# Performance work log

Measured on AMD Instinct MI355X. Metric: run time of the kernel, lower is better.

Reference implementation:

```python
import jax, jax.numpy as jnp
import numpy as np

RATIO = 0.3
BN_EPS = 1e-5
L2_EPS = 1e-8


def setup_inputs() -> dict:
    key = jax.random.key(0)
    ks = jax.random.split(key, 16)
    B, N, D, E = 128, 577, 512, 1024
    H = E // 2  # mlp hidden = 512
    s = lambda k, shp, fan: jax.random.normal(k, shp, dtype=jnp.float32) * (1.0 / np.sqrt(fan))
    return {
        "features": jax.random.normal(ks[0], (B, N, D), dtype=jnp.float32),
        "atten": jax.random.uniform(ks[1], (B, N), dtype=jnp.float32),
        # image_weight_generator: Linear(D,D) -> ReLU -> Linear(D,1)
        "wg_w1": s(ks[2], (D, D), D), "wg_b1": jnp.zeros((D,), jnp.float32),
        "wg_w2": s(ks[3], (D, 1), D), "wg_b2": jnp.zeros((1,), jnp.float32),
        # fc: Linear(D, E)
        "fc_w": s(ks[4], (D, E), D), "fc_b": jnp.zeros((E,), jnp.float32),
        # MLP: Linear(D,H) -> BN(H) -> ReLU -> Linear(H,E)
        "mlp_w0": s(ks[5], (D, H), D), "mlp_b0": jnp.zeros((H,), jnp.float32),
        "bn_g": jnp.ones((H,), jnp.float32), "bn_b": jnp.zeros((H,), jnp.float32),
        "mlp_w1": s(ks[6], (H, E), H), "mlp_b1": jnp.zeros((E,), jnp.float32),
    }


def reference(features, atten, wg_w1, wg_b1, wg_w2, wg_b2, fc_w, fc_b,
              mlp_w0, mlp_b0, bn_g, bn_b, mlp_w1, mlp_b1):
    k = int((atten.shape[1] - 1) * RATIO)  # static: int(576*0.3)=172
    # weight-generator MLP -> per-token scalar weights [B, N]
    h = jax.nn.relu(jnp.einsum('bnd,de->bne', features, wg_w1) + wg_b1)
    w = (jnp.einsum('bnd,do->bno', h, wg_w2) + wg_b2)[..., 0]
    w = w.at[:, 0].set(-jnp.inf)  # mask CLS token
    w = jax.nn.softmax(w, axis=1)
    # top-k token selection (sorted indices), batched gather
    _, idx = jax.lax.top_k(w, k)                      # [B, k]
    idx = jnp.sort(idx, axis=1)
    sel = jnp.take_along_axis(features, idx[:, :, None], axis=1)  # [B, k, D]
    # l2norm over feature dim
    norm = jnp.sqrt(jnp.sum(sel * sel, axis=-1, keepdims=True)) + L2_EPS
    sel = sel / norm
    # fc in half precision (original: fc(selected_tokens.half()))
    feats = (sel.astype(jnp.float16) @ fc_w.astype(jnp.float16)
             + fc_b.astype(jnp.float16))              # [B, k, E] fp16
    # MLP with training-mode BatchNorm over flattened (B*k) dim
    B, K, D = sel.shape
    x = sel.reshape(B * K, D) @ mlp_w0 + mlp_b0       # [B*k, H]
    mean = jnp.mean(x, axis=0)
    var = jnp.mean((x - mean) ** 2, axis=0)
    x = (x - mean) * jax.lax.rsqrt(var + BN_EPS) * bn_g + bn_b
    x = jax.nn.relu(x)
    x = (x @ mlp_w1 + mlp_b1).reshape(B, K, -1)       # [B, k, E]
    return (x + feats.astype(jnp.float32)).astype(jnp.float32)
```

## Files before the change

### kernel.cpp

```cpp
#include <hip/hip_runtime.h>
#include <hip/hip_fp16.h>
#include <math.h>

#define B_    128
#define NTOK  577
#define D_    512
#define E_    1024
#define KSEL  172
#define M_WG  (B_*NTOK)
#define M_SEL (B_*KSEL)

typedef float f32x4 __attribute__((ext_vector_type(4)));
typedef short s16x8 __attribute__((ext_vector_type(8)));
typedef short s16x4 __attribute__((ext_vector_type(4)));

__device__ __forceinline__ unsigned short bf16_rne(float x) {
    unsigned u = __float_as_uint(x);
    u += 0x7FFFu + ((u >> 16) & 1u);
    return (unsigned short)(u >> 16);
}
__device__ __forceinline__ float bf16f(unsigned short h) {
    return __uint_as_float(((unsigned)h) << 16);
}

__global__ void zero_kernel(float* __restrict__ w, float* __restrict__ stats) {
    int i = blockIdx.x * 256 + threadIdx.x;
    if (i < M_WG) w[i] = 0.f;
    if (i < 1024) stats[i] = 0.f;
}

__global__ __launch_bounds__(256) void transpose_split_kernel(
    const float* __restrict__ wgw1, const float* __restrict__ mw0,
    const float* __restrict__ mw1, const float* __restrict__ fcw,
    short* __restrict__ w1t_h, short* __restrict__ w1t_l,
    short* __restrict__ w0t_h, short* __restrict__ w0t_l,
    short* __restrict__ mw1t_h, short* __restrict__ mw1t_l,
    short* __restrict__ fct_h, short* __restrict__ fct_l)
{
    const int z = blockIdx.z;
    const float* src; short *dh, *dl; int N; bool f16r = false;
    if (z == 0)      { src = wgw1; dh = w1t_h;  dl = w1t_l;  N = 512; }
    else if (z == 1) { src = mw0;  dh = w0t_h;  dl = w0t_l;  N = 512; }
    else if (z == 2) { src = mw1;  dh = mw1t_h; dl = mw1t_l; N = 1024; }
    else             { src = fcw;  dh = fct_h;  dl = fct_l;  N = 1024; f16r = true; }
    const int n0 = blockIdx.x * 64;
    if (n0 >= N) return;
    const int k0 = blockIdx.y * 64;
    __shared__ float t[64][65];
    const int tid = threadIdx.x;
#pragma unroll
    for (int rr = 0; rr < 16; rr++) {
        int kl = rr * 4 + (tid >> 6);
        int nl = tid & 63;
        t[kl][nl] = src[(size_t)(k0 + kl) * N + n0 + nl];
    }
    __syncthreads();
    const int nl = tid >> 2, kc = tid & 3;
    short hs[16], ls[16];
#pragma unroll
    for (int j = 0; j < 16; j++) {
        float x = t[kc * 16 + j][nl];
        if (f16r) x = __half2float(__float2half(x));
        unsigned short h = bf16_rne(x);
        hs[j] = (short)h;
        ls[j] = (short)bf16_rne(x - bf16f(h));
    }
    size_t o = (size_t)(n0 + nl) * 512 + k0 + kc * 16;
    *(s16x8*)(dh + o)     = *(s16x8*)hs;
    *(s16x8*)(dh + o + 8) = *(s16x8*)(hs + 8);
    *(s16x8*)(dl + o)     = *(s16x8*)ls;
    *(s16x8*)(dl + o + 8) = *(s16x8*)(ls + 8);
}

__device__ __forceinline__ void stage_bf16(short* dst, const short* __restrict__ src,
                                           int row_base, int k0, int Ktot, int tid)
{
#pragma unroll
    for (int p = 0; p < 2; p++) {
        int c = tid + p * 256;
        int n = c >> 2, kc = c & 3;
        s16x8 v = *(const s16x8*)(src + (size_t)(row_base + n) * Ktot + k0 + kc * 8);
        *(s16x8*)(dst + c * 8) = v;
    }
}

template<bool AFFINE>
__device__ __forceinline__ void stage_f32_split(short* dstH, short* dstL,
    const float* __restrict__ src, int row_base, int k0, int Ktot, int tid,
    const float* sc, const float* sh)
{
#pragma unroll
    for (int p = 0; p < 2; p++) {
        int c = tid + p * 256;
        int n = c >> 2, kc = c & 3;
        const float* s = src + (size_t)(row_base + n) * Ktot + k0 + kc * 8;
        float4 v0 = *(const float4*)(s);
        float4 v1 = *(const float4*)(s + 4);
        float vv[8] = {v0.x, v0.y, v0.z, v0.w, v1.x, v1.y, v1.z, v1.w};
        short hs[8], ls[8];
#pragma unroll
        for (int j = 0; j < 8; j++) {
            float x = vv[j];
            if (AFFINE) {
                int k = k0 + kc * 8 + j;
                x = fmaxf(fmaf(x, sc[k], sh[k]), 0.f);
            }
            unsigned short h = bf16_rne(x);
            hs[j] = (short)h;
            ls[j] = (short)bf16_rne(x - bf16f(h));
        }
        *(s16x8*)(dstH + c * 8) = *(s16x8*)hs;
        *(s16x8*)(dstL + c * 8) = *(s16x8*)ls;
    }
}

__device__ __forceinline__ void mfma_x2_tile(
    const short* Ah, const short* Al, const short* Bh, const short* Bl,
    f32x4 acc[4][4], int wm, int wn, int lane)
{
    const int r = lane & 15, kq = lane >> 4;
    s16x8 ah[4], al[4], bh[4], bl[4];
#pragma unroll
    for (int mf = 0; mf < 4; mf++) {
        int off = (wm * 64 + mf * 16 + r) * 32 + kq * 8;
        ah[mf] = *(const s16x8*)(Ah + off);
        al[mf] = *(const s16x8*)(Al + off);
    }
#pragma unroll
    for (int nf = 0; nf < 4; nf++) {
        int off = (wn * 64 + nf * 16 + r) * 32 + kq * 8;
        bh[nf] = *(const s16x8*)(Bh + off);
        bl[nf] = *(const s16x8*)(Bl + off);
    }
#pragma unroll
    for (int mf = 0; mf < 4; mf++)
#pragma unroll
        for (int nf = 0; nf < 4; nf++) {
            acc[mf][nf] = __builtin_amdgcn_mfma_f32_16x16x32_bf16(ah[mf], bh[nf], acc[mf][nf], 0, 0, 0);
            acc[mf][nf] = __builtin_amdgcn_mfma_f32_16x16x32_bf16(ah[mf], bl[nf], acc[mf][nf], 0, 0, 0);
            acc[mf][nf] = __builtin_amdgcn_mfma_f32_16x16x32_bf16(al[mf], bh[nf], acc[mf][nf], 0, 0, 0);
        }
}

__global__ __launch_bounds__(256) void gemm_wg_kernel(
    const float* __restrict__ F, const short* __restrict__ Wh, const short* __restrict__ Wl,
    const float* __restrict__ b1, const float* __restrict__ v, float* __restrict__ w_out)
{
    __shared__ short Ah[128 * 32], Al[128 * 32], Bh[128 * 32], Bl[128 * 32];
    const int tid = threadIdx.x, lane = tid & 63, w = tid >> 6;
    const int wm = w >> 1, wn = w & 1;
    const int rowbase = blockIdx.y * 128, nbase = blockIdx.x * 128;
    f32x4 acc[4][4];
#pragma unroll
    for (int i = 0; i < 4; i++)
#pragma unroll
        for (int j = 0; j < 4; j++) acc[i][j] = (f32x4)(0.0f);
    for (int k0 = 0; k0 < 512; k0 += 32) {
        stage_f32_split<false>(Ah, Al, F, rowbase, k0, 512, tid, nullptr, nullptr);
        stage_bf16(Bh, Wh, nbase, k0, 512, tid);
        stage_bf16(Bl, Wl, nbase, k0, 512, tid);
        __syncthreads();
        mfma_x2_tile(Ah, Al, Bh, Bl, acc, wm, wn, lane);
        __syncthreads();
    }
    const int r = lane & 15, kq = lane >> 4;
    float b1v[4], vv[4];
#pragma unroll
    for (int nf = 0; nf < 4; nf++) {
        int col = nbase + wn * 64 + nf * 16 + r;
        b1v[nf] = b1[col]; vv[nf] = v[col];
    }
#pragma unroll
    for (int mf = 0; mf < 4; mf++)
#pragma unroll
        for (int i = 0; i < 4; i++) {
            float s = 0.f;
#pragma unroll
            for (int nf = 0; nf < 4; nf++)
                s += fmaxf(acc[mf][nf][i] + b1v[nf], 0.f) * vv[nf];
            s += __shfl_xor(s, 1); s += __shfl_xor(s, 2);
            s += __shfl_xor(s, 4); s += __shfl_xor(s, 8);
            if (r == 0)
                atomicAdd(&w_out[rowbase + wm * 64 + mf * 16 + kq * 4 + i], s);
        }
}

__global__ __launch_bounds__(512) void topk_kernel(
    const float* __restrict__ w, int* __restrict__ idx_out)
{
    __shared__ float sval[1024];
    __shared__ int   sidx[1024];
    __shared__ int   s2[256];
    const int b = blockIdx.x;
    const int tid = threadIdx.x;
    for (int i = tid; i < 1024; i += 512) {
        if (i < 576) { sval[i] = w[b * NTOK + 1 + i]; sidx[i] = 1 + i; }
        else         { sval[i] = -1e38f;              sidx[i] = 0x7fffffff; }
    }
    __syncthreads();
    for (int ksz = 2; ksz <= 1024; ksz <<= 1) {
        for (int j = ksz >> 1; j > 0; j >>= 1) {
            int i = ((tid & ~(j - 1)) << 1) | (tid & (j - 1));
            int ixj = i | j;
            float va = sval[i], vb = sval[ixj];
            int ia = sidx[i], ib = sidx[ixj];
            bool a_first = (va > vb) || (va == vb && ia < ib);
            bool dirDesc = ((i & ksz) == 0);
            bool doswap = dirDesc ? (!a_first) : a_first;
            if (doswap) { sval[i] = vb; sval[ixj] = va; sidx[i] = ib; sidx[ixj] = ia; }
            __syncthreads();
        }
    }
    for (int i = tid; i < 256; i += 512) s2[i] = (i < KSEL) ? sidx[i] : 0x7fffffff;
    __syncthreads();
    for (int ksz = 2; ksz <= 256; ksz <<= 1) {
        for (int j = ksz >> 1; j > 0; j >>= 1) {
            if (tid < 128) {
                int i = ((tid & ~(j - 1)) << 1) | (tid & (j - 1));
                int ixj = i | j;
                int a = s2[i], bb = s2[ixj];
                bool asc = ((i & ksz) == 0);
                bool doswap = asc ? (a > bb) : (a < bb);
                if (doswap) { s2[i] = bb; s2[ixj] = a; }
            }
            __syncthreads();
        }
    }
    for (int i = tid; i < KSEL; i += 512) idx_out[b * KSEL + i] = s2[i];
}

__global__ __launch_bounds__(128) void gather_norm_kernel(
    const float* __restrict__ F, const int* __restrict__ idx,
    short* __restrict__ Sh, short* __restrict__ Sl)
{
    const int g = blockIdx.x;
    const int b = g / KSEL;
    const int tok = idx[g];
    const float4* src = (const float4*)(F + ((size_t)b * NTOK + tok) * 512);
    const int t = threadIdx.x;
    float4 v = src[t];
    float ss = v.x * v.x + v.y * v.y + v.z * v.z + v.w * v.w;
#pragma unroll
    for (int off = 32; off > 0; off >>= 1) ss += __shfl_down(ss, off);
    __shared__ float red[2];
    if ((t & 63) == 0) red[t >> 6] = ss;
    __syncthreads();
    float inv = 1.0f / (sqrtf(red[0] + red[1]) + 1e-8f);
    float xs[4] = {v.x * inv, v.y * inv, v.z * inv, v.w * inv};
    short hs[4], ls[4];
#pragma unroll
    for (int j = 0; j < 4; j++) {
        float x = __half2float(__float2half(xs[j]));
        unsigned short h = bf16_rne(x);
        hs[j] = (short)h;
        ls[j] = (short)bf16_rne(x - bf16f(h));
    }
    *(s16x4*)(Sh + (size_t)g * 512 + t * 4) = *(s16x4*)hs;
    *(s16x4*)(Sl + (size_t)g * 512 + t * 4) = *(s16x4*)ls;
}

__global__ __launch_bounds__(256) void gemm_x1_kernel(
    const short* __restrict__ Sh, const short* __restrict__ Sl,
    const short* __restrict__ Wh, const short* __restrict__ Wl,
    const float* __restrict__ b0, float* __restrict__ X1, float* __restrict__ stats)
{
    __shared__ short Ah[128 * 32], Al[128 * 32], Bh[128 * 32], Bl[128 * 32];
    const int tid = threadIdx.x, lane = tid & 63, w = tid >> 6;
    const int wm = w >> 1, wn = w & 1;
    const int rowbase = blockIdx.y * 128, nbase = blockIdx.x * 128;
    f32x4 acc[4][4];
#pragma unroll
    for (int i = 0; i < 4; i++)
#pragma unroll
        for (int j = 0; j < 4; j++) acc[i][j] = (f32x4)(0.0f);
    for (int k0 = 0; k0 < 512; k0 += 32) {
        stage_bf16(Ah, Sh, rowbase, k0, 512, tid);
        stage_bf16(Al, Sl, rowbase, k0, 512, tid);
        stage_bf16(Bh, Wh, nbase, k0, 512, tid);
        stage_bf16(Bl, Wl, nbase, k0, 512, tid);
        __syncthreads();
        mfma_x2_tile(Ah, Al, Bh, Bl, acc, wm, wn, lane);
        __syncthreads();
    }
    const int r = lane & 15, kq = lane >> 4;
#pragma unroll
    for (int nf = 0; nf < 4; nf++) {
        int col = nbase + wn * 64 + nf * 16 + r;
        float b0v = b0[col];
        float cs = 0.f, cq = 0.f;
#pragma unroll
        for (int mf = 0; mf < 4; mf++)
#pragma unroll
            for (int i = 0; i < 4; i++) {
                int row = rowbase + wm * 64 + mf * 16 + kq * 4 + i;
                float val = acc[mf][nf][i] + b0v;
                X1[(size_t)row * 512 + col] = val;
                cs += val; cq += val * val;
            }
        cs += __shfl_xor(cs, 16); cs += __shfl_xor(cs, 32);
        cq += __shfl_xor(cq, 16); cq += __shfl_xor(cq, 32);
        if (kq == 0) {
            atomicAdd(&stats[col], cs);
            atomicAdd(&stats[512 + col], cq);
        }
    }
}

__global__ void bn_finalize_kernel(const float* __restrict__ stats,
                                   const float* __restrict__ g,
                                   const float* __restrict__ b,
                                   float* __restrict__ ss)
{
    int c = threadIdx.x;
    float mean = stats[c] * (1.0f / M_SEL);
    float var = stats[512 + c] * (1.0f / M_SEL) - mean * mean;
    float sc = g[c] * rsqrtf(var + 1e-5f);
    ss[c] = sc;
    ss[512 + c] = b[c] - mean * sc;
}

__global__ __launch_bounds__(256) void gemm_out2_kernel(
    const short* __restrict__ Sh, const short* __restrict__ Sl,
    const short* __restrict__ FCh, const short* __restrict__ FCl,
    const float* __restrict__ fcb, const float* __restrict__ X1,
    const short* __restrict__ W1h, const short* __restrict__ W1l,
    const float* __restrict__ ssbuf, const float* __restrict__ b1,
    float* __restrict__ out)
{
    __shared__ short Ah[128 * 32], Al[128 * 32], Bh[128 * 32], Bl[128 * 32];
    __shared__ float sc[512], sh_[512];
    const int tid = threadIdx.x, lane = tid & 63, w = tid >> 6;
    const int wm = w >> 1, wn = w & 1;
    const int rowbase = blockIdx.y * 128, nbase = blockIdx.x * 128;
    for (int i = tid; i < 512; i += 256) { sc[i] = ssbuf[i]; sh_[i] = ssbuf[512 + i]; }
    f32x4 acc[4][4];
#pragma unroll
    for (int i = 0; i < 4; i++)
#pragma unroll
        for (int j = 0; j < 4; j++) acc[i][j] = (f32x4)(0.0f);
    for (int k0 = 0; k0 < 512; k0 += 32) {
        stage_bf16(Ah, Sh, rowbase, k0, 512, tid);
        stage_bf16(Al, Sl, rowbase, k0, 512, tid);
        stage_bf16(Bh, FCh, nbase, k0, 512, tid);
        stage_bf16(Bl, FCl, nbase, k0, 512, tid);
        __syncthreads();
        mfma_x2_tile(Ah, Al, Bh, Bl, acc, wm, wn, lane);
        __syncthreads();
    }
    const int r = lane & 15;
#pragma unroll
    for (int nf = 0; nf < 4; nf++) {
        float fb = __half2float(__float2half(fcb[nbase + wn * 64 + nf * 16 + r]));
#pragma unroll
        for (int mf = 0; mf < 4; mf++)
#pragma unroll
            for (int i = 0; i < 4; i++) {
                float t = __half2float(__float2half(acc[mf][nf][i]));
                acc[mf][nf][i] = __half2float(__float2half(t + fb));
            }
    }
    for (int k0 = 0; k0 < 512; k0 += 32) {
        stage_f32_split<true>(Ah, Al, X1, rowbase, k0, 512, tid, sc, sh_);
        stage_bf16(Bh, W1h, nbase, k0, 512, tid);
        stage_bf16(Bl, W1l, nbase, k0, 512, tid);
        __syncthreads();
        mfma_x2_tile(Ah, Al, Bh, Bl, acc, wm, wn, lane);
        __syncthreads();
    }
    const int kq = lane >> 4;
#pragma unroll
    for (int nf = 0; nf < 4; nf++) {
        int col = nbase + wn * 64 + nf * 16 + r;
        float bb = b1[col];
#pragma unroll
        for (int mf = 0; mf < 4; mf++)
#pragma unroll
            for (int i = 0; i < 4; i++) {
                int row = rowbase + wm * 64 + mf * 16 + kq * 4 + i;
                out[(size_t)row * 1024 + col] = acc[mf][nf][i] + bb;
            }
    }
}

extern "C" void kernel_launch(void* const* d_in, const int* in_sizes, int n_in,
                              void* d_out, int out_size, void* d_ws, size_t ws_size,
                              hipStream_t stream)
{
    const float* features = (const float*)d_in[0];
    const float* wg_w1 = (const float*)d_in[2];
    const float* wg_b1 = (const float*)d_in[3];
    const float* wg_w2 = (const float*)d_in[4];
    const float* fc_w  = (const float*)d_in[6];
    const float* fc_b  = (const float*)d_in[7];
    const float* mlp_w0 = (const float*)d_in[8];
    const float* mlp_b0 = (const float*)d_in[9];
    const float* bn_g  = (const float*)d_in[10];
    const float* bn_b  = (const float*)d_in[11];
    const float* mlp_w1 = (const float*)d_in[12];
    const float* mlp_b1 = (const float*)d_in[13];
    float* out = (float*)d_out;

    char* ws = (char*)d_ws;
    float* w_scores  = (float*)(ws + 0);
    float* stats     = (float*)(ws + 295424);
    float* scaleshift= (float*)(ws + 299520);
    int*   idx_sel   = (int*)  (ws + 303616);
    short* w1t_h     = (short*)(ws + 391680);
    short* w1t_l     = (short*)(ws + 915968);
    short* w0t_h     = (short*)(ws + 1440256);
    short* w0t_l     = (short*)(ws + 1964544);
    short* mw1t_h    = (short*)(ws + 2488832);
    short* mw1t_l    = (short*)(ws + 3537408);
    short* fct_h     = (short*)(ws + 4585984);
    short* fct_l     = (short*)(ws + 5634560);
    short* sel_h     = (short*)(ws + 6683136);
    short* sel_l     = (short*)(ws + 29227520);
    float* x1        = (float*)(ws + 51771904);

    zero_kernel<<<289, 256, 0, stream>>>(w_scores, stats);
    transpose_split_kernel<<<dim3(16, 8, 4), 256, 0, stream>>>(
        wg_w1, mlp_w0, mlp_w1, fc_w,
        w1t_h, w1t_l, w0t_h, w0t_l, mw1t_h, mw1t_l, fct_h, fct_l);
    gemm_wg_kernel<<<dim3(4, 577), 256, 0, stream>>>(
        features, w1t_h, w1t_l, wg_b1, wg_w2, w_scores);
    topk_kernel<<<B_, 512, 0, stream>>>(w_scores, idx_sel);
    gather_norm_kernel<<<M_SEL, 128, 0, stream>>>(features, idx_sel, sel_h, sel_l);
    gemm_x1_kernel<<<dim3(4, 172), 256, 0, stream>>>(
        sel_h, sel_l, w0t_h, w0t_l, mlp_b0, x1, stats);
    bn_finalize_kernel<<<1, 512, 0, stream>>>(stats, bn_g, bn_b, scaleshift);
    gemm_out2_kernel<<<dim3(8, 172), 256, 0, stream>>>(
        sel_h, sel_l, fct_h, fct_l, fc_b, x1, mw1t_h, mw1t_l, scaleshift, mlp_b1, out);
}
```

Before: 624.3 us.

## Switch selected-token GEMMs to single-pass fp16 MFMA with direct-to-LDS loads

The downstream GEMMs (x1, fc, mlp second layer) drop the split bf16 hi/lo three-MFMA emulation and run as a single fp16 MFMA pass. The gathered tokens, weights and the x1 intermediate are now stored as fp16, which halves memory traffic and removes the split buffers. The tiles are widened to 128x256 with each wave covering all rows, and operand staging uses global_load_lds. The score GEMM keeps its split-bf16 path but adopts the new k-major LDS layout and direct loads. The risk is lower precision in the MLP branch, where x1 is stored as fp16 and the mlp weights are rounded to fp16, which may shift results relative to the fp32 reference.

```diff
diff --git a/kernel.cpp b/kernel.cpp
--- a/kernel.cpp
+++ b/kernel.cpp
@@ -4,8 +4,6 @@
 
 #define B_    128
 #define NTOK  577
-#define D_    512
-#define E_    1024
 #define KSEL  172
 #define M_WG  (B_*NTOK)
 #define M_SEL (B_*KSEL)
@@ -13,6 +11,7 @@
 typedef float f32x4 __attribute__((ext_vector_type(4)));
 typedef short s16x8 __attribute__((ext_vector_type(8)));
 typedef short s16x4 __attribute__((ext_vector_type(4)));
+typedef _Float16 f16x8 __attribute__((ext_vector_type(8)));
 
 __device__ __forceinline__ unsigned short bf16_rne(float x) {
     unsigned u = __float_as_uint(x);
@@ -22,6 +21,11 @@
 __device__ __forceinline__ float bf16f(unsigned short h) {
     return __uint_as_float(((unsigned)h) << 16);
 }
+__device__ __forceinline__ void gll16(const void* g, void* l) {
+    __builtin_amdgcn_global_load_lds(
+        (const __attribute__((address_space(1))) unsigned int*)g,
+        (__attribute__((address_space(3))) unsigned int*)l, 16, 0, 0);
+}
 
 __global__ void zero_kernel(float* __restrict__ w, float* __restrict__ stats) {
     int i = blockIdx.x * 256 + threadIdx.x;
@@ -33,16 +37,14 @@
     const float* __restrict__ wgw1, const float* __restrict__ mw0,
     const float* __restrict__ mw1, const float* __restrict__ fcw,
     short* __restrict__ w1t_h, short* __restrict__ w1t_l,
-    short* __restrict__ w0t_h, short* __restrict__ w0t_l,
-    short* __restrict__ mw1t_h, short* __restrict__ mw1t_l,
-    short* __restrict__ fct_h, short* __restrict__ fct_l)
+    short* __restrict__ w0t, short* __restrict__ mw1t, short* __restrict__ fct)
 {
     const int z = blockIdx.z;
-    const float* src; short *dh, *dl; int N; bool f16r = false;
-    if (z == 0)      { src = wgw1; dh = w1t_h;  dl = w1t_l;  N = 512; }
-    else if (z == 1) { src = mw0;  dh = w0t_h;  dl = w0t_l;  N = 512; }
-    else if (z == 2) { src = mw1;  dh = mw1t_h; dl = mw1t_l; N = 1024; }
-    else             { src = fcw;  dh = fct_h;  dl = fct_l;  N = 1024; f16r = true; }
+    const float* src; short *dh, *dl = nullptr; int N; int bfmode;
+    if (z == 0)      { src = wgw1; dh = w1t_h; dl = w1t_l; N = 512;  bfmode = 1; }
+    else if (z == 1) { src = mw0;  dh = w0t;   N = 512;  bfmode = 0; }
+    else if (z == 2) { src = mw1;  dh = mw1t;  N = 1024; bfmode = 0; }
+    else             { src = fcw;  dh = fct;   N = 1024; bfmode = 0; }
     const int n0 = blockIdx.x * 64;
     if (n0 >= N) return;
     const int k0 = blockIdx.y * 64;
@@ -60,110 +62,86 @@
 #pragma unroll
     for (int j = 0; j < 16; j++) {
         float x = t[kc * 16 + j][nl];
-        if (f16r) x = __half2float(__float2half(x));
-        unsigned short h = bf16_rne(x);
-        hs[j] = (short)h;
-        ls[j] = (short)bf16_rne(x - bf16f(h));
+        if (bfmode) {
+            unsigned short h = bf16_rne(x);
+            hs[j] = (short)h;
+            ls[j] = (short)bf16_rne(x - bf16f(h));
+        } else {
+            hs[j] = (short)__half_as_ushort(__float2half(x));
+        }
     }
     size_t o = (size_t)(n0 + nl) * 512 + k0 + kc * 16;
     *(s16x8*)(dh + o)     = *(s16x8*)hs;
     *(s16x8*)(dh + o + 8) = *(s16x8*)(hs + 8);
-    *(s16x8*)(dl + o)     = *(s16x8*)ls;
-    *(s16x8*)(dl + o + 8) = *(s16x8*)(ls + 8);
-}
-
-__device__ __forceinline__ void stage_bf16(short* dst, const short* __restrict__ src,
-                                           int row_base, int k0, int Ktot, int tid)
-{
-#pragma unroll
-    for (int p = 0; p < 2; p++) {
-        int c = tid + p * 256;
-        int n = c >> 2, kc = c & 3;
-        s16x8 v = *(const s16x8*)(src + (size_t)(row_base + n) * Ktot + k0 + kc * 8);
-        *(s16x8*)(dst + c * 8) = v;
-    }
-}
-
-template<bool AFFINE>
-__device__ __forceinline__ void stage_f32_split(short* dstH, short* dstL,
-    const float* __restrict__ src, int row_base, int k0, int Ktot, int tid,
-    const float* sc, const float* sh)
-{
-#pragma unroll
-    for (int p = 0; p < 2; p++) {
-        int c = tid + p * 256;
-        int n = c >> 2, kc = c & 3;
-        const float* s = src + (size_t)(row_base + n) * Ktot + k0 + kc * 8;
-        float4 v0 = *(const float4*)(s);
-        float4 v1 = *(const float4*)(s + 4);
-        float vv[8] = {v0.x, v0.y, v0.z, v0.w, v1.x, v1.y, v1.z, v1.w};
-        short hs[8], ls[8];
-#pragma unroll
-        for (int j = 0; j < 8; j++) {
-            float x = vv[j];
-            if (AFFINE) {
-                int k = k0 + kc * 8 + j;
-                x = fmaxf(fmaf(x, sc[k], sh[k]), 0.f);
-            }
-            unsigned short h = bf16_rne(x);
-            hs[j] = (short)h;
-            ls[j] = (short)bf16_rne(x - bf16f(h));
-        }
-        *(s16x8*)(dstH + c * 8) = *(s16x8*)hs;
-        *(s16x8*)(dstL + c * 8) = *(s16x8*)ls;
-    }
-}
-
-__device__ __forceinline__ void mfma_x2_tile(
-    const short* Ah, const short* Al, const short* Bh, const short* Bl,
-    f32x4 acc[4][4], int wm, int wn, int lane)
-{
-    const int r = lane & 15, kq = lane >> 4;
-    s16x8 ah[4], al[4], bh[4], bl[4];
-#pragma unroll
-    for (int mf = 0; mf < 4; mf++) {
-        int off = (wm * 64 + mf * 16 + r) * 32 + kq * 8;
-        ah[mf] = *(const s16x8*)(Ah + off);
-        al[mf] = *(const s16x8*)(Al + off);
-    }
-#pragma unroll
-    for (int nf = 0; nf < 4; nf++) {
-        int off = (wn * 64 + nf * 16 + r) * 32 + kq * 8;
-        bh[nf] = *(const s16x8*)(Bh + off);
-        bl[nf] = *(const s16x8*)(Bl + off);
-    }
-#pragma unroll
-    for (int mf = 0; mf < 4; mf++)
-#pragma unroll
-        for (int nf = 0; nf < 4; nf++) {
-            acc[mf][nf] = __builtin_amdgcn_mfma_f32_16x16x32_bf16(ah[mf], bh[nf], acc[mf][nf], 0, 0, 0);
-            acc[mf][nf] = __builtin_amdgcn_mfma_f32_16x16x32_bf16(ah[mf], bl[nf], acc[mf][nf], 0, 0, 0);
-            acc[mf][nf] = __builtin_amdgcn_mfma_f32_16x16x32_bf16(al[mf], bh[nf], acc[mf][nf], 0, 0, 0);
-        }
+    if (bfmode) {
+        *(s16x8*)(dl + o)     = *(s16x8*)ls;
+        *(s16x8*)(dl + o + 8) = *(s16x8*)(ls + 8);
+    }
 }
 
 __global__ __launch_bounds__(256) void gemm_wg_kernel(
     const float* __restrict__ F, const short* __restrict__ Wh, const short* __restrict__ Wl,
     const float* __restrict__ b1, const float* __restrict__ v, float* __restrict__ w_out)
 {
-    __shared__ short Ah[128 * 32], Al[128 * 32], Bh[128 * 32], Bl[128 * 32];
+    __shared__ short Ah[4096], Al[4096], Bh[4096], Bl[4096];
     const int tid = threadIdx.x, lane = tid & 63, w = tid >> 6;
     const int wm = w >> 1, wn = w & 1;
     const int rowbase = blockIdx.y * 128, nbase = blockIdx.x * 128;
+    const int r = lane & 15, kq = lane >> 4;
     f32x4 acc[4][4];
 #pragma unroll
     for (int i = 0; i < 4; i++)
 #pragma unroll
         for (int j = 0; j < 4; j++) acc[i][j] = (f32x4)(0.0f);
     for (int k0 = 0; k0 < 512; k0 += 32) {
-        stage_f32_split<false>(Ah, Al, F, rowbase, k0, 512, tid, nullptr, nullptr);
-        stage_bf16(Bh, Wh, nbase, k0, 512, tid);
-        stage_bf16(Bl, Wl, nbase, k0, 512, tid);
-        __syncthreads();
-        mfma_x2_tile(Ah, Al, Bh, Bl, acc, wm, wn, lane);
-        __syncthreads();
-    }
-    const int r = lane & 15, kq = lane >> 4;
+#pragma unroll
+        for (int p = 0; p < 2; p++) {
+            int c = tid + p * 256, row = c & 127, kqs = c >> 7;
+            const float* s = F + (size_t)(rowbase + row) * 512 + k0 + kqs * 8;
+            float4 v0 = *(const float4*)s;
+            float4 v1 = *(const float4*)(s + 4);
+            float vv[8] = {v0.x, v0.y, v0.z, v0.w, v1.x, v1.y, v1.z, v1.w};
+            short hs[8], ls[8];
+#pragma unroll
+            for (int j = 0; j < 8; j++) {
+                unsigned short h = bf16_rne(vv[j]);
+                hs[j] = (short)h;
+                ls[j] = (short)bf16_rne(vv[j] - bf16f(h));
+            }
+            *(s16x8*)(Ah + kqs * 1024 + row * 8) = *(s16x8*)hs;
+            *(s16x8*)(Al + kqs * 1024 + row * 8) = *(s16x8*)ls;
+        }
+#pragma unroll
+        for (int p = 0; p < 2; p++) {
+            int c = tid + p * 256, row = c & 127, kqs = c >> 7;
+            size_t go = (size_t)(nbase + row) * 512 + k0 + kqs * 8;
+            gll16(Wh + go, Bh + c * 8);
+            gll16(Wl + go, Bl + c * 8);
+        }
+        __syncthreads();
+        s16x8 ah[4], al[4], bh[4], bl[4];
+#pragma unroll
+        for (int mf = 0; mf < 4; mf++) {
+            int off = kq * 1024 + (wm * 64 + mf * 16 + r) * 8;
+            ah[mf] = *(const s16x8*)(Ah + off);
+            al[mf] = *(const s16x8*)(Al + off);
+        }
+#pragma unroll
+        for (int nf = 0; nf < 4; nf++) {
+            int off = kq * 1024 + (wn * 64 + nf * 16 + r) * 8;
+            bh[nf] = *(const s16x8*)(Bh + off);
+            bl[nf] = *(const s16x8*)(Bl + off);
+        }
+#pragma unroll
+        for (int mf = 0; mf < 4; mf++)
+#pragma unroll
+            for (int nf = 0; nf < 4; nf++) {
+                acc[mf][nf] = __builtin_amdgcn_mfma_f32_16x16x32_bf16(ah[mf], bh[nf], acc[mf][nf], 0, 0, 0);
+                acc[mf][nf] = __builtin_amdgcn_mfma_f32_16x16x32_bf16(ah[mf], bl[nf], acc[mf][nf], 0, 0, 0);
+                acc[mf][nf] = __builtin_amdgcn_mfma_f32_16x16x32_bf16(al[mf], bh[nf], acc[mf][nf], 0, 0, 0);
+            }
+        __syncthreads();
+    }
     float b1v[4], vv[4];
 #pragma unroll
     for (int nf = 0; nf < 4; nf++) {
@@ -231,7 +209,7 @@
 
 __global__ __launch_bounds__(128) void gather_norm_kernel(
     const float* __restrict__ F, const int* __restrict__ idx,
-    short* __restrict__ Sh, short* __restrict__ Sl)
+    short* __restrict__ Sh)
 {
     const int g = blockIdx.x;
     const int b = g / KSEL;
@@ -247,54 +225,62 @@
     __syncthreads();
     float inv = 1.0f / (sqrtf(red[0] + red[1]) + 1e-8f);
     float xs[4] = {v.x * inv, v.y * inv, v.z * inv, v.w * inv};
-    short hs[4], ls[4];
-#pragma unroll
-    for (int j = 0; j < 4; j++) {
-        float x = __half2float(__float2half(xs[j]));
-        unsigned short h = bf16_rne(x);
-        hs[j] = (short)h;
-        ls[j] = (short)bf16_rne(x - bf16f(h));
-    }
+    short hs[4];
+#pragma unroll
+    for (int j = 0; j < 4; j++) hs[j] = (short)__half_as_ushort(__float2half(xs[j]));
     *(s16x4*)(Sh + (size_t)g * 512 + t * 4) = *(s16x4*)hs;
-    *(s16x4*)(Sl + (size_t)g * 512 + t * 4) = *(s16x4*)ls;
 }
 
 __global__ __launch_bounds__(256) void gemm_x1_kernel(
-    const short* __restrict__ Sh, const short* __restrict__ Sl,
-    const short* __restrict__ Wh, const short* __restrict__ Wl,
-    const float* __restrict__ b0, float* __restrict__ X1, float* __restrict__ stats)
-{
-    __shared__ short Ah[128 * 32], Al[128 * 32], Bh[128 * 32], Bl[128 * 32];
-    const int tid = threadIdx.x, lane = tid & 63, w = tid >> 6;
-    const int wm = w >> 1, wn = w & 1;
-    const int rowbase = blockIdx.y * 128, nbase = blockIdx.x * 128;
-    f32x4 acc[4][4];
-#pragma unroll
-    for (int i = 0; i < 4; i++)
+    const short* __restrict__ Sh, const short* __restrict__ W0t,
+    const float* __restrict__ b0, short* __restrict__ X1h, float* __restrict__ stats)
+{
+    __shared__ short A[4096], Bt[8192];
+    const int tid = threadIdx.x, lane = tid & 63, wn = tid >> 6;
+    const int rowbase = blockIdx.y * 128, nbase = blockIdx.x * 256;
+    const int r = lane & 15, kq = lane >> 4;
+    f32x4 acc[8][4];
+#pragma unroll
+    for (int i = 0; i < 8; i++)
 #pragma unroll
         for (int j = 0; j < 4; j++) acc[i][j] = (f32x4)(0.0f);
     for (int k0 = 0; k0 < 512; k0 += 32) {
-        stage_bf16(Ah, Sh, rowbase, k0, 512, tid);
-        stage_bf16(Al, Sl, rowbase, k0, 512, tid);
-        stage_bf16(Bh, Wh, nbase, k0, 512, tid);
-        stage_bf16(Bl, Wl, nbase, k0, 512, tid);
-        __syncthreads();
-        mfma_x2_tile(Ah, Al, Bh, Bl, acc, wm, wn, lane);
-        __syncthreads();
-    }
-    const int r = lane & 15, kq = lane >> 4;
+#pragma unroll
+        for (int p = 0; p < 2; p++) {
+            int c = tid + p * 256, row = c & 127, kqs = c >> 7;
+            gll16(Sh + (size_t)(rowbase + row) * 512 + k0 + kqs * 8, A + c * 8);
+        }
+#pragma unroll
+        for (int p = 0; p < 4; p++) {
+            int c = tid + p * 256, col = c & 255, kqs = c >> 8;
+            gll16(W0t + (size_t)(nbase + col) * 512 + k0 + kqs * 8, Bt + c * 8);
+        }
+        __syncthreads();
+        f16x8 b[4];
+#pragma unroll
+        for (int nf = 0; nf < 4; nf++)
+            b[nf] = *(const f16x8*)(Bt + kq * 2048 + (wn * 64 + nf * 16 + r) * 8);
+#pragma unroll
+        for (int mf = 0; mf < 8; mf++) {
+            f16x8 a = *(const f16x8*)(A + kq * 1024 + (mf * 16 + r) * 8);
+#pragma unroll
+            for (int nf = 0; nf < 4; nf++)
+                acc[mf][nf] = __builtin_amdgcn_mfma_f32_16x16x32_f16(a, b[nf], acc[mf][nf], 0, 0, 0);
+        }
+        __syncthreads();
+    }
 #pragma unroll
     for (int nf = 0; nf < 4; nf++) {
         int col = nbase + wn * 64 + nf * 16 + r;
         float b0v = b0[col];
         float cs = 0.f, cq = 0.f;
 #pragma unroll
-        for (int mf = 0; mf < 4; mf++)
+        for (int mf = 0; mf < 8; mf++)
 #pragma unroll
             for (int i = 0; i < 4; i++) {
-                int row = rowbase + wm * 64 + mf * 16 + kq * 4 + i;
+                int row = rowbase + mf * 16 + kq * 4 + i;
                 float val = acc[mf][nf][i] + b0v;
-                X1[(size_t)row * 512 + col] = val;
+                X1h[(size_t)row * 512 + col] = (short)__half_as_ushort(__float2half(val));
                 cs += val; cq += val * val;
             }
         cs += __shfl_xor(cs, 16); cs += __shfl_xor(cs, 32);
@@ -320,39 +306,52 @@
 }
 
 __global__ __launch_bounds__(256) void gemm_out2_kernel(
-    const short* __restrict__ Sh, const short* __restrict__ Sl,
-    const short* __restrict__ FCh, const short* __restrict__ FCl,
-    const float* __restrict__ fcb, const float* __restrict__ X1,
-    const short* __restrict__ W1h, const short* __restrict__ W1l,
-    const float* __restrict__ ssbuf, const float* __restrict__ b1,
-    float* __restrict__ out)
-{
-    __shared__ short Ah[128 * 32], Al[128 * 32], Bh[128 * 32], Bl[128 * 32];
+    const short* __restrict__ Sh, const short* __restrict__ FCt,
+    const float* __restrict__ fcb, const short* __restrict__ X1h,
+    const short* __restrict__ W1t, const float* __restrict__ ssbuf,
+    const float* __restrict__ b1, float* __restrict__ out)
+{
+    __shared__ short A[4096], Bt[8192];
     __shared__ float sc[512], sh_[512];
-    const int tid = threadIdx.x, lane = tid & 63, w = tid >> 6;
-    const int wm = w >> 1, wn = w & 1;
-    const int rowbase = blockIdx.y * 128, nbase = blockIdx.x * 128;
+    const int tid = threadIdx.x, lane = tid & 63, wn = tid >> 6;
+    const int rowbase = blockIdx.y * 128, nbase = blockIdx.x * 256;
+    const int r = lane & 15, kq = lane >> 4;
     for (int i = tid; i < 512; i += 256) { sc[i] = ssbuf[i]; sh_[i] = ssbuf[512 + i]; }
-    f32x4 acc[4][4];
-#pragma unroll
-    for (int i = 0; i < 4; i++)
+    f32x4 acc[8][4];
+#pragma unroll
+    for (int i = 0; i < 8; i++)
 #pragma unroll
         for (int j = 0; j < 4; j++) acc[i][j] = (f32x4)(0.0f);
     for (int k0 = 0; k0 < 512; k0 += 32) {
-        stage_bf16(Ah, Sh, rowbase, k0, 512, tid);
-        stage_bf16(Al, Sl, rowbase, k0, 512, tid);
-        stage_bf16(Bh, FCh, nbase, k0, 512, tid);
-        stage_bf16(Bl, FCl, nbase, k0, 512, tid);
-        __syncthreads();
-        mfma_x2_tile(Ah, Al, Bh, Bl, acc, wm, wn, lane);
-        __syncthreads();
-    }
-    const int r = lane & 15;
+#pragma unroll
+        for (int p = 0; p < 2; p++) {
+            int c = tid + p * 256, row = c & 127, kqs = c >> 7;
+            gll16(Sh + (size_t)(rowbase + row) * 512 + k0 + kqs * 8, A + c * 8);
+        }
+#pragma unroll
+        for (int p = 0; p < 4; p++) {
+            int c = tid + p * 256, col = c & 255, kqs = c >> 8;
+            gll16(FCt + (size_t)(nbase + col) * 512 + k0 + kqs * 8, Bt + c * 8);
+        }
+        __syncthreads();
+        f16x8 b[4];
+#pragma unroll
+        for (int nf = 0; nf < 4; nf++)
+            b[nf] = *(const f16x8*)(Bt + kq * 2048 + (wn * 64 + nf * 16 + r) * 8);
+#pragma unroll
+        for (int mf = 0; mf < 8; mf++) {
+            f16x8 a = *(const f16x8*)(A + kq * 1024 + (mf * 16 + r) * 8);
+#pragma unroll
+            for (int nf = 0; nf < 4; nf++)
+                acc[mf][nf] = __builtin_amdgcn_mfma_f32_16x16x32_f16(a, b[nf], acc[mf][nf], 0, 0, 0);
+        }
+        __syncthreads();
+    }
 #pragma unroll
     for (int nf = 0; nf < 4; nf++) {
         float fb = __half2float(__float2half(fcb[nbase + wn * 64 + nf * 16 + r]));
 #pragma unroll
-        for (int mf = 0; mf < 4; mf++)
+        for (int mf = 0; mf < 8; mf++)
 #pragma unroll
             for (int i = 0; i < 4; i++) {
                 float t = __half2float(__float2half(acc[mf][nf][i]));
@@ -360,23 +359,48 @@
             }
     }
     for (int k0 = 0; k0 < 512; k0 += 32) {
-        stage_f32_split<true>(Ah, Al, X1, rowbase, k0, 512, tid, sc, sh_);
-        stage_bf16(Bh, W1h, nbase, k0, 512, tid);
-        stage_bf16(Bl, W1l, nbase, k0, 512, tid);
-        __syncthreads();
-        mfma_x2_tile(Ah, Al, Bh, Bl, acc, wm, wn, lane);
-        __syncthreads();
-    }
-    const int kq = lane >> 4;
+#pragma unroll
+        for (int p = 0; p < 2; p++) {
+            int c = tid + p * 256, row = c & 127, kqs = c >> 7;
+            s16x8 xi = *(const s16x8*)(X1h + (size_t)(rowbase + row) * 512 + k0 + kqs * 8);
+            short hs[8];
+#pragma unroll
+            for (int j = 0; j < 8; j++) {
+                float xf = __half2float(__ushort_as_half((unsigned short)xi[j]));
+                int k = k0 + kqs * 8 + j;
+                float y = fmaxf(fmaf(xf, sc[k], sh_[k]), 0.f);
+                hs[j] = (short)__half_as_ushort(__float2half(y));
+            }
+            *(s16x8*)(A + kqs * 1024 + row * 8) = *(s16x8*)hs;
+        }
+#pragma unroll
+        for (int p = 0; p < 4; p++) {
+            int c = tid + p * 256, col = c & 255, kqs = c >> 8;
+            gll16(W1t + (size_t)(nbase + col) * 512 + k0 + kqs * 8, Bt + c * 8);
+        }
+        __syncthreads();
+        f16x8 b[4];
+#pragma unroll
+        for (int nf = 0; nf < 4; nf++)
+            b[nf] = *(const f16x8*)(Bt + kq * 2048 + (wn * 64 + nf * 16 + r) * 8);
+#pragma unroll
+        for (int mf = 0; mf < 8; mf++) {
+            f16x8 a = *(const f16x8*)(A + kq * 1024 + (mf * 16 + r) * 8);
+#pragma unroll
+            for (int nf = 0; nf < 4; nf++)
+                acc[mf][nf] = __builtin_amdgcn_mfma_f32_16x16x32_f16(a, b[nf], acc[mf][nf], 0, 0, 0);
+        }
+        __syncthreads();
+    }
 #pragma unroll
     for (int nf = 0; nf < 4; nf++) {
         int col = nbase + wn * 64 + nf * 16 + r;
         float bb = b1[col];
 #pragma unroll
-        for (int mf = 0; mf < 4; mf++)
+        for (int mf = 0; mf < 8; mf++)
 #pragma unroll
             for (int i = 0; i < 4; i++) {
-                int row = rowbase + wm * 64 + mf * 16 + kq * 4 + i;
+                int row = rowbase + mf * 16 + kq * 4 + i;
                 out[(size_t)row * 1024 + col] = acc[mf][nf][i] + bb;
             }
     }
@@ -407,27 +431,22 @@
     int*   idx_sel   = (int*)  (ws + 303616);
     short* w1t_h     = (short*)(ws + 391680);
     short* w1t_l     = (short*)(ws + 915968);
-    short* w0t_h     = (short*)(ws + 1440256);
-    short* w0t_l     = (short*)(ws + 1964544);
-    short* mw1t_h    = (short*)(ws + 2488832);
-    short* mw1t_l    = (short*)(ws + 3537408);
-    short* fct_h     = (short*)(ws + 4585984);
-    short* fct_l     = (short*)(ws + 5634560);
-    short* sel_h     = (short*)(ws + 6683136);
-    short* sel_l     = (short*)(ws + 29227520);
-    float* x1        = (float*)(ws + 51771904);
+    short* w0t       = (short*)(ws + 1440256);
+    short* mw1t      = (short*)(ws + 1964544);
+    short* fct       = (short*)(ws + 3013120);
+    short* sel_h     = (short*)(ws + 4061696);
+    short* x1h       = (short*)(ws + 26606080);
 
     zero_kernel<<<289, 256, 0, stream>>>(w_scores, stats);
     transpose_split_kernel<<<dim3(16, 8, 4), 256, 0, stream>>>(
-        wg_w1, mlp_w0, mlp_w1, fc_w,
-        w1t_h, w1t_l, w0t_h, w0t_l, mw1t_h, mw1t_l, fct_h, fct_l);
+        wg_w1, mlp_w0, mlp_w1, fc_w, w1t_h, w1t_l, w0t, mw1t, fct);
     gemm_wg_kernel<<<dim3(4, 577), 256, 0, stream>>>(
         features, w1t_h, w1t_l, wg_b1, wg_w2, w_scores);
     topk_kernel<<<B_, 512, 0, stream>>>(w_scores, idx_sel);
-    gather_norm_kernel<<<M_SEL, 128, 0, stream>>>(features, idx_sel, sel_h, sel_l);
-    gemm_x1_kernel<<<dim3(4, 172), 256, 0, stream>>>(
-        sel_h, sel_l, w0t_h, w0t_l, mlp_b0, x1, stats);
+    gather_norm_kernel<<<M_SEL, 128, 0, stream>>>(features, idx_sel, sel_h);
+    gemm_x1_kernel<<<dim3(2, 172), 256, 0, stream>>>(
+        sel_h, w0t, mlp_b0, x1h, stats);
     bn_finalize_kernel<<<1, 512, 0, stream>>>(stats, bn_g, bn_b, scaleshift);
-    gemm_out2_kernel<<<dim3(8, 172), 256, 0, stream>>>(
-        sel_h, sel_l, fct_h, fct_l, fc_b, x1, mw1t_h, mw1t_l, scaleshift, mlp_b1, out);
-}
+    gemm_out2_kernel<<<dim3(4, 172), 256, 0, stream>>>(
+        sel_h, fct, fc_b, x1h, mw1t, scaleshift, mlp_b1, out);
+}
```

Result: slower. 688.0 us (+10.2%).
